# Optimization experiments

Measured on AMD Instinct MI355X. Metric: run time of the kernel, lower is better.

The kernel has to match this reference:

```python
import jax, jax.numpy as jnp
import numpy as np

B, INDIM, OUTDIM = 1024, 2048, 4096


def setup_inputs() -> dict:
    key = jax.random.key(0)
    kx, kw, kb = jax.random.split(key, 3)
    x = jax.random.normal(kx, (B, INDIM), dtype=jnp.float32)
    # nn.Linear(indim, outdim): weight [outdim, indim], bias [outdim]
    bound = 1.0 / np.sqrt(INDIM)
    W = jax.random.uniform(kw, (OUTDIM, INDIM), minval=-bound, maxval=bound, dtype=jnp.float32)
    b = jax.random.uniform(kb, (OUTDIM,), minval=-bound, maxval=bound, dtype=jnp.float32)
    return {"x": x, "W": W, "b": b}


def reference(x, W, b):
    # Faithful to torch: prototypes = weight.transpose(0,1).reshape(outdim, indim)
    # (a reflatten of W^T, not the original weight rows, since outdim != indim).
    protos = W.T.reshape(W.shape[0], W.shape[1])  # [outdim, indim]
    # -||x_i - p_j||^2 - b_j via GEMM identity (same math as broadcast subtract + norm^2)
    x_sq = jnp.sum(x * x, axis=1, keepdims=True)          # [B, 1]
    p_sq = jnp.sum(protos * protos, axis=1)[None, :]      # [1, outdim]
    xp = jnp.einsum('bd,od->bo', x, protos)               # [B, outdim]
    return -(x_sq - 2.0 * xp + p_sq) - b[None, :]
```

## Files before the change

kernel.cpp:

```cpp
#include <hip/hip_runtime.h>

#define IN_DIM  2048
#define OUT_DIM 4096

typedef float     f32x4 __attribute__((ext_vector_type(4)));
typedef long long llx2  __attribute__((ext_vector_type(2)));

__device__ __forceinline__ unsigned int pk4(float a, float b, float c, float d) {
    int v = __builtin_amdgcn_cvt_pk_fp8_f32(a, b, 0, false);
    v     = __builtin_amdgcn_cvt_pk_fp8_f32(c, d, v, true);
    return (unsigned int)v;
}

__device__ __forceinline__ void async16(const void* g, void* l) {
    __builtin_amdgcn_global_load_lds(
        (const __attribute__((address_space(1))) unsigned int*)g,
        (__attribute__((address_space(3))) unsigned int*)l,
        16, 0, 0);
}

__device__ __forceinline__ int gmem_of(int c) { return 2 * (c & 3) + (c >> 2); }

extern "C" __global__ __launch_bounds__(256) void transpose_w(
        const float* __restrict__ W, unsigned char* __restrict__ protos,
        float* __restrict__ psq) {
    __shared__ float tile[64][65];
    const int r  = blockIdx.z;
    const int c0 = blockIdx.x * 64;
    const int d0 = blockIdx.y * 64;
    const int t  = threadIdx.x;
    const int g  = t >> 4;
    const int cc = (t & 15) * 4;

    const float* Wp = W + (size_t)(r * IN_DIM + d0 + g) * IN_DIM + c0 + cc;
#pragma unroll
    for (int p = 0; p < 4; ++p) {
        const float4 v = *(const float4*)(Wp + (size_t)(16 * p) * IN_DIM);
        const int dl = g + 16 * p;
        tile[dl][cc]     = v.x;
        tile[dl][cc + 1] = v.y;
        tile[dl][cc + 2] = v.z;
        tile[dl][cc + 3] = v.w;
    }
    __syncthreads();

    const int c8 = t & 7;
    const int gm = gmem_of(c8);
#pragma unroll
    for (int p = 0; p < 2; ++p) {
        const int cr = (t >> 3) + 32 * p;
        float v[8];
        float ss = 0.f;
#pragma unroll
        for (int j = 0; j < 8; ++j) {
            v[j] = tile[8 * c8 + j][cr];
            ss += v[j] * v[j];
        }
        const int o = 2 * (c0 + cr) + r;
        uint2 pk;
        pk.x = pk4(16.f * v[0], 16.f * v[1], 16.f * v[2], 16.f * v[3]);
        pk.y = pk4(16.f * v[4], 16.f * v[5], 16.f * v[6], 16.f * v[7]);
        *(uint2*)(protos + (size_t)o * IN_DIM + d0 + gm * 8) = pk;
        ss += __shfl_xor(ss, 1);
        ss += __shfl_xor(ss, 2);
        ss += __shfl_xor(ss, 4);
        if (c8 == 0) atomicAdd(psq + o, ss);
    }
}

extern "C" __global__ __launch_bounds__(256) void xcast_xsq(
        const float* __restrict__ x,
        unsigned char* __restrict__ xb,
        float* __restrict__ x_sq,
        float* __restrict__ psq) {
    __shared__ float red[4];
    const int b = blockIdx.x;
    const int t = threadIdx.x;
    if (t < 4) psq[b * 4 + t] = 0.f;
    const float* xp = x + (size_t)b * IN_DIM + t * 8;
    const float4 v0 = ((const float4*)xp)[0];
    const float4 v1 = ((const float4*)xp)[1];
    uint2 pk;
    pk.x = pk4(v0.x, v0.y, v0.z, v0.w);
    pk.y = pk4(v1.x, v1.y, v1.z, v1.w);
    *(uint2*)(xb + (size_t)b * IN_DIM + (t >> 3) * 64 + gmem_of(t & 7) * 8) = pk;

    float s = v0.x * v0.x + v0.y * v0.y + v0.z * v0.z + v0.w * v0.w
            + v1.x * v1.x + v1.y * v1.y + v1.z * v1.z + v1.w * v1.w;
#pragma unroll
    for (int off = 32; off > 0; off >>= 1) s += __shfl_down(s, off);
    const int lane = t & 63, w = t >> 6;
    if (lane == 0) red[w] = s;
    __syncthreads();
    if (t == 0) x_sq[b] = red[0] + red[1] + red[2] + red[3];
}

extern "C" __global__ __launch_bounds__(256, 4) void gemm_epi(
        const unsigned char* __restrict__ A,
        const unsigned char* __restrict__ Bt,
        const float* __restrict__ x_sq,
        const float* __restrict__ psq,
        const float* __restrict__ bias,
        float* __restrict__ out) {
    __shared__ __align__(16) unsigned char smem[16384];
    unsigned char* lA = smem;
    unsigned char* lB = smem + 8192;

    const int lid = blockIdx.x;
    const int xcd = lid & 7;
    const int wi  = lid >> 3;
    const int nt  = xcd * 8 + (wi & 7);
    const int mt  = wi >> 3;
    const int m0 = mt * 64;
    const int n0 = nt * 64;

    const int t = threadIdx.x;
    const int rS = t >> 3;
    const int pS = t & 7;
    const int lS = pS ^ (rS & 7);
    const size_t goff = (size_t)(lS >> 2) * 1024 + (lS & 3) * 16;
    const unsigned char* gA0 = A  + (size_t)(m0 + rS) * IN_DIM + goff;
    const unsigned char* gA1 = gA0 + (size_t)32 * IN_DIM;
    const unsigned char* gB0 = Bt + (size_t)(n0 + rS) * IN_DIM + goff;
    const unsigned char* gB1 = gB0 + (size_t)32 * IN_DIM;
    unsigned char* lAd = lA + t * 16;
    unsigned char* lBd = lB + t * 16;

    const int wave = t >> 6;
    const int lane = t & 63;
    const int kh = wave & 1;
    const int nh = wave >> 1;
    const int ln = lane & 15;
    const int qd = lane >> 4;
    const int pr = (kh * 4 + qd) ^ (ln & 7);

    f32x4 acc[4][2] = {};

    for (int it = 0; it < 16; ++it) {
        async16(gA0, lAd); async16(gA1, lAd + 4096);
        async16(gB0, lBd); async16(gB1, lBd + 4096);
        gA0 += 64; gA1 += 64; gB0 += 64; gB1 += 64;
        __syncthreads();

        llx2 af[4], bf[2];
#pragma unroll
        for (int i = 0; i < 4; ++i)
            af[i] = *(const llx2*)(lA + (i * 16 + ln) * 128 + pr * 16);
#pragma unroll
        for (int j = 0; j < 2; ++j)
            bf[j] = *(const llx2*)(lB + (nh * 32 + j * 16 + ln) * 128 + pr * 16);
#pragma unroll
        for (int kk = 0; kk < 2; ++kk)
#pragma unroll
            for (int i = 0; i < 4; ++i)
#pragma unroll
                for (int j = 0; j < 2; ++j)
                    acc[i][j] = __builtin_amdgcn_mfma_f32_16x16x32_fp8_fp8(
                                    af[i][kk], bf[j][kk], acc[i][j], 0, 0, 0);
        __syncthreads();
    }

    if (kh == 1) {
#pragma unroll
        for (int i = 0; i < 4; ++i)
#pragma unroll
            for (int j = 0; j < 2; ++j)
                *(f32x4*)(smem + nh * 8192 + (i * 2 + j) * 1024 + lane * 16) =
                    acc[i][j];
    }
    __syncthreads();
    if (kh == 0) {
        const int rowb = m0;
        const int colb = n0 + nh * 32;
#pragma unroll
        for (int j = 0; j < 2; ++j) {
            const int col = colb + j * 16 + ln;
            const float pb = psq[col] + bias[col];
#pragma unroll
            for (int i = 0; i < 4; ++i) {
                const f32x4 o4 = *(const f32x4*)(smem + nh * 8192 +
                                                 (i * 2 + j) * 1024 + lane * 16);
                const int row0 = rowb + i * 16 + qd * 4;
#pragma unroll
                for (int rr = 0; rr < 4; ++rr) {
                    const int row = row0 + rr;
                    out[(size_t)row * OUT_DIM + col] =
                        0.125f * (acc[i][j][rr] + o4[rr]) - x_sq[row] - pb;
                }
            }
        }
    }
}

extern "C" void kernel_launch(void* const* d_in, const int* in_sizes, int n_in,
                              void* d_out, int out_size, void* d_ws, size_t ws_size,
                              hipStream_t stream) {
    const float* x    = (const float*)d_in[0];
    const float* W    = (const float*)d_in[1];
    const float* bias = (const float*)d_in[2];
    float* out = (float*)d_out;

    char* ws = (char*)d_ws;
    unsigned char* protos = (unsigned char*)ws;
    unsigned char* xb     = (unsigned char*)(ws + (size_t)8 * 1024 * 1024);
    float* x_sq           = (float*)(ws + (size_t)10 * 1024 * 1024);
    float* psq            = (float*)(ws + (size_t)10 * 1024 * 1024 + 8192);

    xcast_xsq<<<dim3(1024), 256, 0, stream>>>(x, xb, x_sq, psq);
    transpose_w<<<dim3(32, 32, 2), 256, 0, stream>>>(W, protos, psq);
    gemm_epi<<<dim3(1024), 256, 0, stream>>>(xb, protos, x_sq, psq, bias, out);
}
```

Measured before the change: 109.1 us.

## Use 16x16x128 scaled FP8 MFMA, merge prep kernels, drop psq atomics

Replaces the 16x16x32 fp8 MFMA with the gfx950 scaled 16x16x128 f8f6f4 MFMA using neutral scales. K-tiles grow to 128 bytes, which doubles LDS to 32KB and changes the swizzle and layout. The x-cast and W-transpose kernels are merged into one launch, and atomic psq accumulation becomes per-tile partial sums that the GEMM epilogue reduces (32 loads per column). This cuts one launch, the atomics and the MFMA issue count, at the cost of more LDS per block, which may lower occupancy, and extra epilogue loads.

```diff
diff --git a/kernel.cpp b/kernel.cpp
--- a/kernel.cpp
+++ b/kernel.cpp
@@ -3,8 +3,9 @@
 #define IN_DIM  2048
 #define OUT_DIM 4096
 
-typedef float     f32x4 __attribute__((ext_vector_type(4)));
-typedef long long llx2  __attribute__((ext_vector_type(2)));
+typedef float f32x4 __attribute__((ext_vector_type(4)));
+typedef int   i32x8 __attribute__((ext_vector_type(8)));
+typedef int   i32x4 __attribute__((ext_vector_type(4)));
 
 __device__ __forceinline__ unsigned int pk4(float a, float b, float c, float d) {
     int v = __builtin_amdgcn_cvt_pk_fp8_f32(a, b, 0, false);
@@ -19,16 +20,37 @@
         16, 0, 0);
 }
 
-__device__ __forceinline__ int gmem_of(int c) { return 2 * (c & 3) + (c >> 2); }
-
-extern "C" __global__ __launch_bounds__(256) void transpose_w(
-        const float* __restrict__ W, unsigned char* __restrict__ protos,
-        float* __restrict__ psq) {
+extern "C" __global__ __launch_bounds__(256) void prep(
+        const float* __restrict__ W, const float* __restrict__ x,
+        unsigned char* __restrict__ protos, unsigned char* __restrict__ xb,
+        float* __restrict__ psq_part, float* __restrict__ x_sq) {
     __shared__ float tile[64][65];
+    const int t = threadIdx.x;
+
+    if (blockIdx.z == 2) {
+        const int b = blockIdx.x + 32 * blockIdx.y;
+        const float* xp = x + (size_t)b * IN_DIM + t * 8;
+        const float4 v0 = ((const float4*)xp)[0];
+        const float4 v1 = ((const float4*)xp)[1];
+        uint2 pk;
+        pk.x = pk4(v0.x, v0.y, v0.z, v0.w);
+        pk.y = pk4(v1.x, v1.y, v1.z, v1.w);
+        *(uint2*)(xb + (size_t)b * IN_DIM + t * 8) = pk;
+
+        float s = v0.x * v0.x + v0.y * v0.y + v0.z * v0.z + v0.w * v0.w
+                + v1.x * v1.x + v1.y * v1.y + v1.z * v1.z + v1.w * v1.w;
+#pragma unroll
+        for (int off = 32; off > 0; off >>= 1) s += __shfl_down(s, off);
+        const int lane = t & 63, w = t >> 6;
+        if (lane == 0) tile[0][w] = s;
+        __syncthreads();
+        if (t == 0) x_sq[b] = tile[0][0] + tile[0][1] + tile[0][2] + tile[0][3];
+        return;
+    }
+
     const int r  = blockIdx.z;
     const int c0 = blockIdx.x * 64;
     const int d0 = blockIdx.y * 64;
-    const int t  = threadIdx.x;
     const int g  = t >> 4;
     const int cc = (t & 15) * 4;
 
@@ -45,7 +67,6 @@
     __syncthreads();
 
     const int c8 = t & 7;
-    const int gm = gmem_of(c8);
 #pragma unroll
     for (int p = 0; p < 2; ++p) {
         const int cr = (t >> 3) + 32 * p;
@@ -60,51 +81,24 @@
         uint2 pk;
         pk.x = pk4(16.f * v[0], 16.f * v[1], 16.f * v[2], 16.f * v[3]);
         pk.y = pk4(16.f * v[4], 16.f * v[5], 16.f * v[6], 16.f * v[7]);
-        *(uint2*)(protos + (size_t)o * IN_DIM + d0 + gm * 8) = pk;
+        *(uint2*)(protos + (size_t)o * IN_DIM + d0 + c8 * 8) = pk;
         ss += __shfl_xor(ss, 1);
         ss += __shfl_xor(ss, 2);
         ss += __shfl_xor(ss, 4);
-        if (c8 == 0) atomicAdd(psq + o, ss);
-    }
-}
-
-extern "C" __global__ __launch_bounds__(256) void xcast_xsq(
-        const float* __restrict__ x,
-        unsigned char* __restrict__ xb,
-        float* __restrict__ x_sq,
-        float* __restrict__ psq) {
-    __shared__ float red[4];
-    const int b = blockIdx.x;
-    const int t = threadIdx.x;
-    if (t < 4) psq[b * 4 + t] = 0.f;
-    const float* xp = x + (size_t)b * IN_DIM + t * 8;
-    const float4 v0 = ((const float4*)xp)[0];
-    const float4 v1 = ((const float4*)xp)[1];
-    uint2 pk;
-    pk.x = pk4(v0.x, v0.y, v0.z, v0.w);
-    pk.y = pk4(v1.x, v1.y, v1.z, v1.w);
-    *(uint2*)(xb + (size_t)b * IN_DIM + (t >> 3) * 64 + gmem_of(t & 7) * 8) = pk;
-
-    float s = v0.x * v0.x + v0.y * v0.y + v0.z * v0.z + v0.w * v0.w
-            + v1.x * v1.x + v1.y * v1.y + v1.z * v1.z + v1.w * v1.w;
-#pragma unroll
-    for (int off = 32; off > 0; off >>= 1) s += __shfl_down(s, off);
-    const int lane = t & 63, w = t >> 6;
-    if (lane == 0) red[w] = s;
-    __syncthreads();
-    if (t == 0) x_sq[b] = red[0] + red[1] + red[2] + red[3];
+        if (c8 == 0) psq_part[(size_t)blockIdx.y * OUT_DIM + o] = ss;
+    }
 }
 
 extern "C" __global__ __launch_bounds__(256, 4) void gemm_epi(
         const unsigned char* __restrict__ A,
         const unsigned char* __restrict__ Bt,
         const float* __restrict__ x_sq,
-        const float* __restrict__ psq,
+        const float* __restrict__ psq_part,
         const float* __restrict__ bias,
         float* __restrict__ out) {
-    __shared__ __align__(16) unsigned char smem[16384];
+    __shared__ __align__(16) unsigned char smem[32768];
     unsigned char* lA = smem;
-    unsigned char* lB = smem + 8192;
+    unsigned char* lB = smem + 16384;
 
     const int lid = blockIdx.x;
     const int xcd = lid & 7;
@@ -115,16 +109,11 @@
     const int n0 = nt * 64;
 
     const int t = threadIdx.x;
-    const int rS = t >> 3;
-    const int pS = t & 7;
-    const int lS = pS ^ (rS & 7);
-    const size_t goff = (size_t)(lS >> 2) * 1024 + (lS & 3) * 16;
-    const unsigned char* gA0 = A  + (size_t)(m0 + rS) * IN_DIM + goff;
-    const unsigned char* gA1 = gA0 + (size_t)32 * IN_DIM;
-    const unsigned char* gB0 = Bt + (size_t)(n0 + rS) * IN_DIM + goff;
-    const unsigned char* gB1 = gB0 + (size_t)32 * IN_DIM;
-    unsigned char* lAd = lA + t * 16;
-    unsigned char* lBd = lB + t * 16;
+    const int rS = t >> 4;
+    const int lS = (t & 15) ^ rS;
+    const size_t gof = (size_t)(lS >> 3) * 1024 + (size_t)(lS & 7) * 16;
+    const unsigned char* gA = A  + (size_t)(m0 + rS) * IN_DIM + gof;
+    const unsigned char* gB = Bt + (size_t)(n0 + rS) * IN_DIM + gof;
 
     const int wave = t >> 6;
     const int lane = t & 63;
@@ -132,31 +121,46 @@
     const int nh = wave >> 1;
     const int ln = lane & 15;
     const int qd = lane >> 4;
-    const int pr = (kh * 4 + qd) ^ (ln & 7);
+    const int cA = kh * 8 + qd * 2;
+    const int p0 = cA ^ ln;
+    const int p1 = (cA + 1) ^ ln;
 
     f32x4 acc[4][2] = {};
 
-    for (int it = 0; it < 16; ++it) {
-        async16(gA0, lAd); async16(gA1, lAd + 4096);
-        async16(gB0, lBd); async16(gB1, lBd + 4096);
-        gA0 += 64; gA1 += 64; gB0 += 64; gB1 += 64;
+    for (int it = 0; it < 8; ++it) {
+#pragma unroll
+        for (int j = 0; j < 4; ++j) {
+            async16(gA + (size_t)(16 * j) * IN_DIM + it * 128,
+                    lA + t * 16 + j * 4096);
+            async16(gB + (size_t)(16 * j) * IN_DIM + it * 128,
+                    lB + t * 16 + j * 4096);
+        }
         __syncthreads();
 
-        llx2 af[4], bf[2];
+        i32x8 af[4], bf[2];
+#pragma unroll
+        for (int i = 0; i < 4; ++i) {
+            const unsigned char* rp = lA + (i * 16 + ln) * 256;
+            const i32x4 lo = *(const i32x4*)(rp + p0 * 16);
+            const i32x4 hi = *(const i32x4*)(rp + p1 * 16);
+            af[i] = __builtin_shufflevector(lo, hi, 0, 1, 2, 3, 4, 5, 6, 7);
+        }
+#pragma unroll
+        for (int j = 0; j < 2; ++j) {
+            const unsigned char* rp = lB + (nh * 32 + j * 16 + ln) * 256;
+            const i32x4 lo = *(const i32x4*)(rp + p0 * 16);
+            const i32x4 hi = *(const i32x4*)(rp + p1 * 16);
+            bf[j] = __builtin_shufflevector(lo, hi, 0, 1, 2, 3, 4, 5, 6, 7);
+        }
 #pragma unroll
         for (int i = 0; i < 4; ++i)
-            af[i] = *(const llx2*)(lA + (i * 16 + ln) * 128 + pr * 16);
-#pragma unroll
-        for (int j = 0; j < 2; ++j)
-            bf[j] = *(const llx2*)(lB + (nh * 32 + j * 16 + ln) * 128 + pr * 16);
-#pragma unroll
-        for (int kk = 0; kk < 2; ++kk)
-#pragma unroll
-            for (int i = 0; i < 4; ++i)
-#pragma unroll
-                for (int j = 0; j < 2; ++j)
-                    acc[i][j] = __builtin_amdgcn_mfma_f32_16x16x32_fp8_fp8(
-                                    af[i][kk], bf[j][kk], acc[i][j], 0, 0, 0);
+#pragma unroll
+            for (int j = 0; j < 2; ++j)
+                acc[i][j] = __builtin_amdgcn_mfma_scale_f32_16x16x128_f8f6f4(
+                                af[i], bf[j], acc[i][j],
+                                0, 0,
+                                0, 127,
+                                0, 127);
         __syncthreads();
     }
 
@@ -170,17 +174,18 @@
     }
     __syncthreads();
     if (kh == 0) {
-        const int rowb = m0;
-        const int colb = n0 + nh * 32;
 #pragma unroll
         for (int j = 0; j < 2; ++j) {
-            const int col = colb + j * 16 + ln;
-            const float pb = psq[col] + bias[col];
+            const int col = n0 + nh * 32 + j * 16 + ln;
+            float pb = bias[col];
+#pragma unroll
+            for (int dt = 0; dt < 32; ++dt)
+                pb += psq_part[(size_t)dt * OUT_DIM + col];
 #pragma unroll
             for (int i = 0; i < 4; ++i) {
                 const f32x4 o4 = *(const f32x4*)(smem + nh * 8192 +
                                                  (i * 2 + j) * 1024 + lane * 16);
-                const int row0 = rowb + i * 16 + qd * 4;
+                const int row0 = m0 + i * 16 + qd * 4;
 #pragma unroll
                 for (int rr = 0; rr < 4; ++rr) {
                     const int row = row0 + rr;
@@ -204,9 +209,8 @@
     unsigned char* protos = (unsigned char*)ws;
     unsigned char* xb     = (unsigned char*)(ws + (size_t)8 * 1024 * 1024);
     float* x_sq           = (float*)(ws + (size_t)10 * 1024 * 1024);
-    float* psq            = (float*)(ws + (size_t)10 * 1024 * 1024 + 8192);
-
-    xcast_xsq<<<dim3(1024), 256, 0, stream>>>(x, xb, x_sq, psq);
-    transpose_w<<<dim3(32, 32, 2), 256, 0, stream>>>(W, protos, psq);
-    gemm_epi<<<dim3(1024), 256, 0, stream>>>(xb, protos, x_sq, psq, bias, out);
-}
+    float* psq_part       = (float*)(ws + (size_t)10 * 1024 * 1024 + 65536);
+
+    prep<<<dim3(32, 32, 3), 256, 0, stream>>>(W, x, protos, xb, psq_part, x_sq);
+    gemm_epi<<<dim3(1024), 256, 0, stream>>>(xb, protos, x_sq, psq_part, bias, out);
+}
```

New measurement: 112.7 us. 1.03x slower.

## Merge x-cast and W-transpose into one prep kernel, replace psq atomics with partials

Applied to the files above, without the earlier changes.

Folds the x fp8-cast/x_sq kernel into the W transpose kernel as an extra grid z-slice, removing one kernel launch and the dependency between them. The per-prototype squared-norm atomics are replaced by plain stores of 32 partial sums per column, which the GEMM epilogue then reduces. This removes the atomic traffic and the zero-init step, but adds 32 extra global loads per column in every GEMM block's epilogue.

```diff
diff --git a/kernel.cpp b/kernel.cpp
--- a/kernel.cpp
+++ b/kernel.cpp
@@ -21,14 +21,37 @@
 
 __device__ __forceinline__ int gmem_of(int c) { return 2 * (c & 3) + (c >> 2); }
 
-extern "C" __global__ __launch_bounds__(256) void transpose_w(
-        const float* __restrict__ W, unsigned char* __restrict__ protos,
-        float* __restrict__ psq) {
+extern "C" __global__ __launch_bounds__(256) void prep(
+        const float* __restrict__ W, const float* __restrict__ x,
+        unsigned char* __restrict__ protos, unsigned char* __restrict__ xb,
+        float* __restrict__ psq_part, float* __restrict__ x_sq) {
     __shared__ float tile[64][65];
+    const int t = threadIdx.x;
+
+    if (blockIdx.z == 2) {
+        const int b = blockIdx.x + 32 * blockIdx.y;
+        const float* xp = x + (size_t)b * IN_DIM + t * 8;
+        const float4 v0 = ((const float4*)xp)[0];
+        const float4 v1 = ((const float4*)xp)[1];
+        uint2 pk;
+        pk.x = pk4(v0.x, v0.y, v0.z, v0.w);
+        pk.y = pk4(v1.x, v1.y, v1.z, v1.w);
+        *(uint2*)(xb + (size_t)b * IN_DIM + (t >> 3) * 64 + gmem_of(t & 7) * 8) = pk;
+
+        float s = v0.x * v0.x + v0.y * v0.y + v0.z * v0.z + v0.w * v0.w
+                + v1.x * v1.x + v1.y * v1.y + v1.z * v1.z + v1.w * v1.w;
+#pragma unroll
+        for (int off = 32; off > 0; off >>= 1) s += __shfl_down(s, off);
+        const int lane = t & 63, w = t >> 6;
+        if (lane == 0) tile[0][w] = s;
+        __syncthreads();
+        if (t == 0) x_sq[b] = tile[0][0] + tile[0][1] + tile[0][2] + tile[0][3];
+        return;
+    }
+
     const int r  = blockIdx.z;
     const int c0 = blockIdx.x * 64;
     const int d0 = blockIdx.y * 64;
-    const int t  = threadIdx.x;
     const int g  = t >> 4;
     const int cc = (t & 15) * 4;
 
@@ -64,42 +87,15 @@
         ss += __shfl_xor(ss, 1);
         ss += __shfl_xor(ss, 2);
         ss += __shfl_xor(ss, 4);
-        if (c8 == 0) atomicAdd(psq + o, ss);
-    }
-}
-
-extern "C" __global__ __launch_bounds__(256) void xcast_xsq(
-        const float* __restrict__ x,
-        unsigned char* __restrict__ xb,
-        float* __restrict__ x_sq,
-        float* __restrict__ psq) {
-    __shared__ float red[4];
-    const int b = blockIdx.x;
-    const int t = threadIdx.x;
-    if (t < 4) psq[b * 4 + t] = 0.f;
-    const float* xp = x + (size_t)b * IN_DIM + t * 8;
-    const float4 v0 = ((const float4*)xp)[0];
-    const float4 v1 = ((const float4*)xp)[1];
-    uint2 pk;
-    pk.x = pk4(v0.x, v0.y, v0.z, v0.w);
-    pk.y = pk4(v1.x, v1.y, v1.z, v1.w);
-    *(uint2*)(xb + (size_t)b * IN_DIM + (t >> 3) * 64 + gmem_of(t & 7) * 8) = pk;
-
-    float s = v0.x * v0.x + v0.y * v0.y + v0.z * v0.z + v0.w * v0.w
-            + v1.x * v1.x + v1.y * v1.y + v1.z * v1.z + v1.w * v1.w;
-#pragma unroll
-    for (int off = 32; off > 0; off >>= 1) s += __shfl_down(s, off);
-    const int lane = t & 63, w = t >> 6;
-    if (lane == 0) red[w] = s;
-    __syncthreads();
-    if (t == 0) x_sq[b] = red[0] + red[1] + red[2] + red[3];
+        if (c8 == 0) psq_part[(size_t)blockIdx.y * OUT_DIM + o] = ss;
+    }
 }
 
 extern "C" __global__ __launch_bounds__(256, 4) void gemm_epi(
         const unsigned char* __restrict__ A,
         const unsigned char* __restrict__ Bt,
         const float* __restrict__ x_sq,
-        const float* __restrict__ psq,
+        const float* __restrict__ psq_part,
         const float* __restrict__ bias,
         float* __restrict__ out) {
     __shared__ __align__(16) unsigned char smem[16384];
@@ -170,17 +166,18 @@
     }
     __syncthreads();
     if (kh == 0) {
-        const int rowb = m0;
-        const int colb = n0 + nh * 32;
 #pragma unroll
         for (int j = 0; j < 2; ++j) {
-            const int col = colb + j * 16 + ln;
-            const float pb = psq[col] + bias[col];
+            const int col = n0 + nh * 32 + j * 16 + ln;
+            float pb = bias[col];
+#pragma unroll
+            for (int dt = 0; dt < 32; ++dt)
+                pb += psq_part[(size_t)dt * OUT_DIM + col];
 #pragma unroll
             for (int i = 0; i < 4; ++i) {
                 const f32x4 o4 = *(const f32x4*)(smem + nh * 8192 +
                                                  (i * 2 + j) * 1024 + lane * 16);
-                const int row0 = rowb + i * 16 + qd * 4;
+                const int row0 = m0 + i * 16 + qd * 4;
 #pragma unroll
                 for (int rr = 0; rr < 4; ++rr) {
                     const int row = row0 + rr;
@@ -204,9 +201,8 @@
     unsigned char* protos = (unsigned char*)ws;
     unsigned char* xb     = (unsigned char*)(ws + (size_t)8 * 1024 * 1024);
     float* x_sq           = (float*)(ws + (size_t)10 * 1024 * 1024);
-    float* psq            = (float*)(ws + (size_t)10 * 1024 * 1024 + 8192);
-
-    xcast_xsq<<<dim3(1024), 256, 0, stream>>>(x, xb, x_sq, psq);
-    transpose_w<<<dim3(32, 32, 2), 256, 0, stream>>>(W, protos, psq);
-    gemm_epi<<<dim3(1024), 256, 0, stream>>>(xb, protos, x_sq, psq, bias, out);
-}
+    float* psq_part       = (float*)(ws + (size_t)10 * 1024 * 1024 + 65536);
+
+    prep<<<dim3(32, 32, 3), 256, 0, stream>>>(W, x, protos, xb, psq_part, x_sq);
+    gemm_epi<<<dim3(1024), 256, 0, stream>>>(xb, protos, x_sq, psq_part, bias, out);
+}
```

New measurement: 106.7 us, median of 2. 2.2% less time.
